# Kernel optimization log

Measured on AMD Instinct MI355X. Metric: run time of the kernel, lower is better.

The kernel has to match this reference:

```python
import jax, jax.numpy as jnp
import numpy as np


def setup_inputs() -> dict:
    key = jax.random.key(0)
    k1, k2 = jax.random.split(key)
    h = jax.random.normal(k1, (8, 16, 64, 512), dtype=jnp.float32)
    M = jax.random.normal(k2, (20000, 512), dtype=jnp.float32)
    return {"h": h, "M": M}


def reference(h, M):
    # h: [B, T, X, R], M: [K, R]
    B, T, X, R = h.shape
    hf = h.reshape(-1, R)                      # [N, R]
    att = jax.nn.softmax(hf @ M.T, axis=1)     # [N, K], unscaled dot-product
    out = att @ M                              # [N, R]
    return out.reshape(B, T, X, R)
```

## Files before the change

### kernel.cpp

```cpp
#include <hip/hip_runtime.h>
#include <stdint.h>

#define NQ 8192
#define NK 20000
#define RD 512
#define NT 157
#define TS0 79

typedef float f32x4 __attribute__((ext_vector_type(4)));
typedef short s16x8 __attribute__((ext_vector_type(8)));

__device__ __forceinline__ unsigned short bf16_rn(float x) {
    uint32_t u = __float_as_uint(x);
    return (unsigned short)((u + 0x7FFFu + ((u >> 16) & 1)) >> 16);
}

__device__ __forceinline__ void lds_barrier() {
    asm volatile("s_waitcnt lgkmcnt(0)\n\ts_barrier" ::: "memory");
}

__global__ void preconv_kernel(const float* __restrict__ M,
                               unsigned short* __restrict__ Mhi,
                               unsigned short* __restrict__ Mlo,
                               unsigned short* __restrict__ MT) {
    __shared__ float tilef[64 * 65];
    const int k0 = blockIdx.x * 64, r0 = blockIdx.y * 64;
    const int t = threadIdx.x;
#pragma unroll
    for (int i = 0; i < 16; i++) {
        int e = t + i * 256;
        int kr = e >> 6, cc = e & 63;
        int key = k0 + kr;
        if (key < NK) {
            float x = M[(size_t)key * RD + r0 + cc];
            uint32_t u = __float_as_uint(x);
            Mhi[(size_t)key * RD + r0 + cc] = (unsigned short)(u >> 16);
            Mlo[(size_t)key * RD + r0 + cc] = bf16_rn(x - __uint_as_float(u & 0xFFFF0000u));
            tilef[cc * 65 + kr] = x;
        }
    }
    __syncthreads();
#pragma unroll
    for (int i = 0; i < 16; i++) {
        int e = t + i * 256;
        int rr = e >> 6, kk = e & 63;
        int key = k0 + kk;
        if (key < NK) MT[(size_t)(r0 + rr) * NK + key] = bf16_rn(tilef[rr * 65 + kk]);
    }
}

#define S_STEP(ii, s_) do {                                                                        \
        const int sl_ = (s_) & 3;                                                                  \
        s16x8 kh0_ = kh[0][sl_], kl0_ = kl[0][sl_];                                                \
        s16x8 kh1_ = kh[1][sl_], kl1_ = kl[1][sl_];                                                \
        {                                                                                          \
            int g_ = (ii) * 16 + (s_) + 4;                                                         \
            size_t a0_ = kaddr(g_, 0), a1_ = kaddr(g_, 1);                                         \
            kh[0][sl_] = *(const s16x8*)(Mhi + a0_);                                               \
            kl[0][sl_] = *(const s16x8*)(Mlo + a0_);                                               \
            kh[1][sl_] = *(const s16x8*)(Mhi + a1_);                                               \
            kl[1][sl_] = *(const s16x8*)(Mlo + a1_);                                               \
        }                                                                                          \
        _Pragma("unroll")                                                                          \
        for (int st_ = 0; st_ < 2; st_++) {                                                        \
            s16x8 qh_ = *(const s16x8*)&qbuf[(st_ * 16 + (s_)) * 512 + l * 8];                     \
            s16x8 ql_ = *(const s16x8*)&qbuf[16384 + (st_ * 16 + (s_)) * 512 + l * 8];             \
            Cc[st_][0] = __builtin_amdgcn_mfma_f32_16x16x32_bf16(qh_, kh0_, Cc[st_][0], 0, 0, 0);  \
            Cc[st_][1] = __builtin_amdgcn_mfma_f32_16x16x32_bf16(qh_, kh1_, Cc[st_][1], 0, 0, 0);  \
            Cc[st_][0] = __builtin_amdgcn_mfma_f32_16x16x32_bf16(ql_, kh0_, Cc[st_][0], 0, 0, 0);  \
            Cc[st_][1] = __builtin_amdgcn_mfma_f32_16x16x32_bf16(ql_, kh1_, Cc[st_][1], 0, 0, 0);  \
            Cc[st_][0] = __builtin_amdgcn_mfma_f32_16x16x32_bf16(qh_, kl0_, Cc[st_][0], 0, 0, 0);  \
            Cc[st_][1] = __builtin_amdgcn_mfma_f32_16x16x32_bf16(qh_, kl1_, Cc[st_][1], 0, 0, 0);  \
        }                                                                                          \
    } while (0)

__global__ __launch_bounds__(256, 2) void flash7_kernel(
        const float* __restrict__ h,
        const unsigned short* __restrict__ Mhi,
        const unsigned short* __restrict__ Mlo,
        const unsigned short* __restrict__ MT,
        float* __restrict__ out,
        float* __restrict__ Opart,
        float* __restrict__ mpart,
        float* __restrict__ lpart,
        int nsplit) {
    __shared__ unsigned short qbuf[32768];
    __shared__ unsigned short pbuf[8 * 512];
    __shared__ float smaxb[4 * 2 * 16];
    __shared__ float ssumb[4 * 2 * 16];

    const int tid = threadIdx.x;
    const int ch = tid >> 6, l = tid & 63;
    const int l15 = l & 15, q4 = l >> 4;
    const int kq = (l15 >> 3) & 1, jj = l15 & 7;

    int qb, split;
    if (nsplit == 2) { split = blockIdx.x & 1; qb = blockIdx.x >> 1; }
    else             { split = 0;              qb = blockIdx.x; }
    const int koff = (split == 0) ? 0 : TS0 * 128;
    const int ntl  = (nsplit == 2) ? ((split == 0) ? TS0 : (NT - TS0)) : NT;
    const int total_ks = ntl * 16;
    const int qbase = qb * 32;

    const size_t base_w = (size_t)(ch * 32 + l15) * RD + q4 * 8;
    auto kaddr = [&](int g, int cb) -> size_t {
        if (g >= total_ks) g = total_ks - 1;
        int t2 = g >> 4, s2 = g & 15;
        return (size_t)(koff + t2 * 128) * RD + (size_t)s2 * 32 + base_w + (size_t)cb * (16 * RD);
    };

    s16x8 kh[2][4], kl[2][4];
#pragma unroll
    for (int i = 0; i < 4; i++) {
        size_t a0 = kaddr(i, 0), a1 = kaddr(i, 1);
        kh[0][i] = *(const s16x8*)(Mhi + a0);
        kl[0][i] = *(const s16x8*)(Mlo + a0);
        kh[1][i] = *(const s16x8*)(Mhi + a1);
        kl[1][i] = *(const s16x8*)(Mlo + a1);
    }

#pragma unroll
    for (int i = 0; i < 8; i++) {
        int g = tid + i * 256;
        int row = g >> 6, s = (g >> 2) & 15, qg = g & 3;
        int strip = row >> 4, lrow = row & 15;
        const float* src = h + (size_t)(qbase + row) * RD + s * 32 + qg * 8;
        f32x4 a = *(const f32x4*)src;
        f32x4 b = *(const f32x4*)(src + 4);
        s16x8 hi8, lo8;
#pragma unroll
        for (int j = 0; j < 8; j++) {
            float x = (j < 4) ? a[j] : b[j - 4];
            uint32_t u = __float_as_uint(x);
            hi8[j] = (short)(u >> 16);
            lo8[j] = (short)bf16_rn(x - __uint_as_float(u & 0xFFFF0000u));
        }
        int off = ((strip * 16 + s) * 512 + (qg * 16 + lrow) * 8);
        *(s16x8*)&qbuf[off] = hi8;
        *(s16x8*)&qbuf[16384 + off] = lo8;
    }
    lds_barrier();

    f32x4 O[2][8];
#pragma unroll
    for (int st = 0; st < 2; st++)
#pragma unroll
        for (int ct = 0; ct < 8; ct++) O[st][ct] = 0.f;
    f32x4 m_run[2], l_run[2];
    m_run[0] = -3e38f; m_run[1] = -3e38f; l_run[0] = 0.f; l_run[1] = 0.f;

    f32x4 Cc[2][2];
    Cc[0][0] = 0.f; Cc[0][1] = 0.f; Cc[1][0] = 0.f; Cc[1][1] = 0.f;
#pragma unroll
    for (int s = 0; s < 16; s++) S_STEP(0, s);

    for (int i = 1; i < ntl; i++) {
        const int prv = i - 1;

        f32x4 Cp[2][2];
#pragma unroll
        for (int st = 0; st < 2; st++) {
            Cp[st][0] = Cc[st][0]; Cp[st][1] = Cc[st][1];
            Cc[st][0] = 0.f;       Cc[st][1] = 0.f;
        }

        const unsigned short* mtp = MT + (size_t)(ch * 128 + l15) * NK + koff + prv * 128 + q4 * 8;
        s16x8 bt[2][4];
#pragma unroll
        for (int sk = 0; sk < 4; sk++) {
            bt[0][sk] = *(const s16x8*)(mtp + sk * 32);
            bt[1][sk] = *(const s16x8*)(mtp + (size_t)16 * NK + sk * 32);
        }
        f32x4 mx[2];
#pragma unroll
        for (int st = 0; st < 2; st++)
#pragma unroll
            for (int v = 0; v < 4; v++) mx[st][v] = fmaxf(Cp[st][0][v], Cp[st][1][v]);
#pragma unroll
        for (int d = 1; d < 16; d <<= 1) {
#pragma unroll
            for (int st = 0; st < 2; st++)
#pragma unroll
                for (int v = 0; v < 4; v++) mx[st][v] = fmaxf(mx[st][v], __shfl_xor(mx[st][v], d, 16));
        }
        if (l15 == 0) {
            *(f32x4*)&smaxb[(ch * 2 + 0) * 16 + q4 * 4] = mx[0];
            *(f32x4*)&smaxb[(ch * 2 + 1) * 16 + q4 * 4] = mx[1];
        }
#pragma unroll
        for (int s = 0; s < 5; s++) S_STEP(i, s);
        lds_barrier();

        f32x4 mnew[2]; mnew[0] = m_run[0]; mnew[1] = m_run[1];
#pragma unroll
        for (int cc = 0; cc < 4; cc++) {
#pragma unroll
            for (int st = 0; st < 2; st++) {
                f32x4 tv = *(const f32x4*)&smaxb[(cc * 2 + st) * 16 + q4 * 4];
#pragma unroll
                for (int v = 0; v < 4; v++) mnew[st][v] = fmaxf(mnew[st][v], tv[v]);
            }
        }
        f32x4 alpha[2];
#pragma unroll
        for (int st = 0; st < 2; st++)
#pragma unroll
            for (int v = 0; v < 4; v++) {
                alpha[st][v] = __expf(m_run[st][v] - mnew[st][v]);
                m_run[st][v] = mnew[st][v];
            }
        f32x4 ps[2]; ps[0] = 0.f; ps[1] = 0.f;
#pragma unroll
        for (int st = 0; st < 2; st++) {
#pragma unroll
            for (int cb = 0; cb < 2; cb++) {
#pragma unroll
                for (int v = 0; v < 4; v++) {
                    float p = __expf(Cp[st][cb][v] - mnew[st][v]);
                    ps[st][v] += p;
                    pbuf[(ch * 2 + st) * 512 + ((cb * 2 + kq) * 16 + q4 * 4 + v) * 8 + jj] = bf16_rn(p);
                }
            }
        }
#pragma unroll
        for (int d = 1; d < 16; d <<= 1) {
#pragma unroll
            for (int st = 0; st < 2; st++)
#pragma unroll
                for (int v = 0; v < 4; v++) ps[st][v] += __shfl_xor(ps[st][v], d, 16);
        }
        if (l15 == 0) {
            *(f32x4*)&ssumb[(ch * 2 + 0) * 16 + q4 * 4] = ps[0];
            *(f32x4*)&ssumb[(ch * 2 + 1) * 16 + q4 * 4] = ps[1];
        }
#pragma unroll
        for (int s = 5; s < 11; s++) S_STEP(i, s);
        lds_barrier();

        f32x4 ts[2]; ts[0] = 0.f; ts[1] = 0.f;
#pragma unroll
        for (int cc = 0; cc < 4; cc++) {
            ts[0] += *(const f32x4*)&ssumb[(cc * 2 + 0) * 16 + q4 * 4];
            ts[1] += *(const f32x4*)&ssumb[(cc * 2 + 1) * 16 + q4 * 4];
        }
#pragma unroll
        for (int st = 0; st < 2; st++)
#pragma unroll
            for (int v = 0; v < 4; v++) l_run[st][v] = l_run[st][v] * alpha[st][v] + ts[st][v];
#pragma unroll
        for (int st = 0; st < 2; st++)
#pragma unroll
            for (int ct = 0; ct < 8; ct++)
#pragma unroll
                for (int v = 0; v < 4; v++) O[st][ct][v] *= alpha[st][v];
        s16x8 pa[2][4];
#pragma unroll
        for (int st = 0; st < 2; st++)
#pragma unroll
            for (int sk = 0; sk < 4; sk++)
                pa[st][sk] = *(const s16x8*)&pbuf[((sk * 2 + st) * 512) + l * 8];
#pragma unroll
        for (int s = 11; s < 16; s++) S_STEP(i, s);
#pragma unroll
        for (int ct = 0; ct < 8; ct++) {
            s16x8 b0 = bt[ct & 1][0], b1 = bt[ct & 1][1], b2 = bt[ct & 1][2], b3 = bt[ct & 1][3];
            if (ct < 6) {
#pragma unroll
                for (int sk = 0; sk < 4; sk++)
                    bt[ct & 1][sk] = *(const s16x8*)(mtp + (size_t)(ct + 2) * 16 * NK + sk * 32);
            }
            O[0][ct] = __builtin_amdgcn_mfma_f32_16x16x32_bf16(pa[0][0], b0, O[0][ct], 0, 0, 0);
            O[1][ct] = __builtin_amdgcn_mfma_f32_16x16x32_bf16(pa[1][0], b0, O[1][ct], 0, 0, 0);
            O[0][ct] = __builtin_amdgcn_mfma_f32_16x16x32_bf16(pa[0][1], b1, O[0][ct], 0, 0, 0);
            O[1][ct] = __builtin_amdgcn_mfma_f32_16x16x32_bf16(pa[1][1], b1, O[1][ct], 0, 0, 0);
            O[0][ct] = __builtin_amdgcn_mfma_f32_16x16x32_bf16(pa[0][2], b2, O[0][ct], 0, 0, 0);
            O[1][ct] = __builtin_amdgcn_mfma_f32_16x16x32_bf16(pa[1][2], b2, O[1][ct], 0, 0, 0);
            O[0][ct] = __builtin_amdgcn_mfma_f32_16x16x32_bf16(pa[0][3], b3, O[0][ct], 0, 0, 0);
            O[1][ct] = __builtin_amdgcn_mfma_f32_16x16x32_bf16(pa[1][3], b3, O[1][ct], 0, 0, 0);
        }
    }

    {
        const int prv = ntl - 1;
#pragma unroll
        for (int cb = 0; cb < 2; cb++) {
            int kg = koff + prv * 128 + ch * 32 + cb * 16 + l15;
            if (kg >= NK) { Cc[0][cb] = -3e38f; Cc[1][cb] = -3e38f; }
        }
        const unsigned short* mtp = MT + (size_t)(ch * 128 + l15) * NK + koff + prv * 128 + q4 * 8;
        s16x8 bt[2][4];
#pragma unroll
        for (int sk = 0; sk < 4; sk++) {
            bt[0][sk] = *(const s16x8*)(mtp + sk * 32);
            bt[1][sk] = *(const s16x8*)(mtp + (size_t)16 * NK + sk * 32);
        }
        f32x4 mx[2];
#pragma unroll
        for (int st = 0; st < 2; st++)
#pragma unroll
            for (int v = 0; v < 4; v++) mx[st][v] = fmaxf(Cc[st][0][v], Cc[st][1][v]);
#pragma unroll
        for (int d = 1; d < 16; d <<= 1) {
#pragma unroll
            for (int st = 0; st < 2; st++)
#pragma unroll
                for (int v = 0; v < 4; v++) mx[st][v] = fmaxf(mx[st][v], __shfl_xor(mx[st][v], d, 16));
        }
        if (l15 == 0) {
            *(f32x4*)&smaxb[(ch * 2 + 0) * 16 + q4 * 4] = mx[0];
            *(f32x4*)&smaxb[(ch * 2 + 1) * 16 + q4 * 4] = mx[1];
        }
        lds_barrier();
        f32x4 mnew[2]; mnew[0] = m_run[0]; mnew[1] = m_run[1];
#pragma unroll
        for (int cc = 0; cc < 4; cc++) {
#pragma unroll
            for (int st = 0; st < 2; st++) {
                f32x4 tv = *(const f32x4*)&smaxb[(cc * 2 + st) * 16 + q4 * 4];
#pragma unroll
                for (int v = 0; v < 4; v++) mnew[st][v] = fmaxf(mnew[st][v], tv[v]);
            }
        }
        f32x4 alpha[2];
#pragma unroll
        for (int st = 0; st < 2; st++)
#pragma unroll
            for (int v = 0; v < 4; v++) {
                alpha[st][v] = __expf(m_run[st][v] - mnew[st][v]);
                m_run[st][v] = mnew[st][v];
            }
        f32x4 ps[2]; ps[0] = 0.f; ps[1] = 0.f;
#pragma unroll
        for (int st = 0; st < 2; st++) {
#pragma unroll
            for (int cb = 0; cb < 2; cb++) {
#pragma unroll
                for (int v = 0; v < 4; v++) {
                    float p = __expf(Cc[st][cb][v] - mnew[st][v]);
                    ps[st][v] += p;
                    pbuf[(ch * 2 + st) * 512 + ((cb * 2 + kq) * 16 + q4 * 4 + v) * 8 + jj] = bf16_rn(p);
                }
            }
        }
#pragma unroll
        for (int d = 1; d < 16; d <<= 1) {
#pragma unroll
            for (int st = 0; st < 2; st++)
#pragma unroll
                for (int v = 0; v < 4; v++) ps[st][v] += __shfl_xor(ps[st][v], d, 16);
        }
        if (l15 == 0) {
            *(f32x4*)&ssumb[(ch * 2 + 0) * 16 + q4 * 4] = ps[0];
            *(f32x4*)&ssumb[(ch * 2 + 1) * 16 + q4 * 4] = ps[1];
        }
        lds_barrier();
        f32x4 ts[2]; ts[0] = 0.f; ts[1] = 0.f;
#pragma unroll
        for (int cc = 0; cc < 4; cc++) {
            ts[0] += *(const f32x4*)&ssumb[(cc * 2 + 0) * 16 + q4 * 4];
            ts[1] += *(const f32x4*)&ssumb[(cc * 2 + 1) * 16 + q4 * 4];
        }
#pragma unroll
        for (int st = 0; st < 2; st++)
#pragma unroll
            for (int v = 0; v < 4; v++) l_run[st][v] = l_run[st][v] * alpha[st][v] + ts[st][v];
#pragma unroll
        for (int st = 0; st < 2; st++)
#pragma unroll
            for (int ct = 0; ct < 8; ct++)
#pragma unroll
                for (int v = 0; v < 4; v++) O[st][ct][v] *= alpha[st][v];
        s16x8 pa[2][4];
#pragma unroll
        for (int st = 0; st < 2; st++)
#pragma unroll
            for (int sk = 0; sk < 4; sk++)
                pa[st][sk] = *(const s16x8*)&pbuf[((sk * 2 + st) * 512) + l * 8];
#pragma unroll
        for (int ct = 0; ct < 8; ct++) {
            s16x8 b0 = bt[ct & 1][0], b1 = bt[ct & 1][1], b2 = bt[ct & 1][2], b3 = bt[ct & 1][3];
            if (ct < 6) {
#pragma unroll
                for (int sk = 0; sk < 4; sk++)
                    bt[ct & 1][sk] = *(const s16x8*)(mtp + (size_t)(ct + 2) * 16 * NK + sk * 32);
            }
            O[0][ct] = __builtin_amdgcn_mfma_f32_16x16x32_bf16(pa[0][0], b0, O[0][ct], 0, 0, 0);
            O[1][ct] = __builtin_amdgcn_mfma_f32_16x16x32_bf16(pa[1][0], b0, O[1][ct], 0, 0, 0);
            O[0][ct] = __builtin_amdgcn_mfma_f32_16x16x32_bf16(pa[0][1], b1, O[0][ct], 0, 0, 0);
            O[1][ct] = __builtin_amdgcn_mfma_f32_16x16x32_bf16(pa[1][1], b1, O[1][ct], 0, 0, 0);
            O[0][ct] = __builtin_amdgcn_mfma_f32_16x16x32_bf16(pa[0][2], b2, O[0][ct], 0, 0, 0);
            O[1][ct] = __builtin_amdgcn_mfma_f32_16x16x32_bf16(pa[1][2], b2, O[1][ct], 0, 0, 0);
            O[0][ct] = __builtin_amdgcn_mfma_f32_16x16x32_bf16(pa[0][3], b3, O[0][ct], 0, 0, 0);
            O[1][ct] = __builtin_amdgcn_mfma_f32_16x16x32_bf16(pa[1][3], b3, O[1][ct], 0, 0, 0);
        }
    }

    if (nsplit == 2) {
        float* Od = Opart + (size_t)split * NQ * RD;
#pragma unroll
        for (int st = 0; st < 2; st++)
#pragma unroll
            for (int ct = 0; ct < 8; ct++)
#pragma unroll
                for (int v = 0; v < 4; v++)
                    Od[(size_t)(qbase + st * 16 + q4 * 4 + v) * RD + ch * 128 + ct * 16 + l15] =
                        O[st][ct][v];
        if (ch == 0 && l15 == 0) {
#pragma unroll
            for (int st = 0; st < 2; st++)
#pragma unroll
                for (int v = 0; v < 4; v++) {
                    mpart[split * NQ + qbase + st * 16 + q4 * 4 + v] = m_run[st][v];
                    lpart[split * NQ + qbase + st * 16 + q4 * 4 + v] = l_run[st][v];
                }
        }
    } else {
#pragma unroll
        for (int st = 0; st < 2; st++)
#pragma unroll
            for (int ct = 0; ct < 8; ct++)
#pragma unroll
                for (int v = 0; v < 4; v++)
                    out[(size_t)(qbase + st * 16 + q4 * 4 + v) * RD + ch * 128 + ct * 16 + l15] =
                        O[st][ct][v] / l_run[st][v];
    }
}

__global__ __launch_bounds__(256) void combine_kernel(const float* __restrict__ Opart,
                                                      const float* __restrict__ mpart,
                                                      const float* __restrict__ lpart,
                                                      float* __restrict__ out) {
    const int t = threadIdx.x;
    const int row = blockIdx.x * 2 + (t >> 7);
    const int d = (t & 127) * 4;
    float m0 = mpart[row], m1 = mpart[NQ + row];
    float l0 = lpart[row], l1 = lpart[NQ + row];
    float m = fmaxf(m0, m1);
    float w0 = __expf(m0 - m), w1 = __expf(m1 - m);
    float inv = 1.f / (w0 * l0 + w1 * l1);
    f32x4 o0 = *(const f32x4*)&Opart[(size_t)row * RD + d];
    f32x4 o1 = *(const f32x4*)&Opart[(size_t)NQ * RD + (size_t)row * RD + d];
    f32x4 r;
#pragma unroll
    for (int v = 0; v < 4; v++) r[v] = (o0[v] * w0 + o1[v] * w1) * inv;
    *(f32x4*)&out[(size_t)row * RD + d] = r;
}

__global__ __launch_bounds__(256) void naive_kernel(const float* __restrict__ h,
                                                    const float* __restrict__ M,
                                                    float* __restrict__ out) {
    __shared__ float hs[16 * 520];
    __shared__ float ms[8 * 520];
    __shared__ float sdot[2][128];
    __shared__ float sm[16], sl[16], sal[16], sp[16][8];
    const int t = threadIdx.x;
    const int qbase = blockIdx.x * 16;
#pragma unroll
    for (int i = 0; i < 32; i++) {
        int e = t + i * 256;
        int row = e >> 9, col = e & 511;
        hs[row * 520 + col] = h[(size_t)(qbase + row) * RD + col];
    }
    if (t < 16) { sm[t] = -3e38f; sl[t] = 0.f; }
    float Oacc[32];
#pragma unroll
    for (int i = 0; i < 32; i++) Oacc[i] = 0.f;
    const int q = t >> 4;
    const int eb = (t & 15) * 32;

    for (int k0 = 0; k0 < NK; k0 += 8) {
        __syncthreads();
#pragma unroll
        for (int i = 0; i < 16; i++) {
            int e = t + i * 256;
            if (e < 4096) {
                int kk = e >> 9, col = e & 511;
                ms[kk * 520 + col] = M[(size_t)(k0 + kk) * RD + col];
            }
        }
        __syncthreads();
        {
            int pair = t & 127, half = t >> 7;
            int qq = pair & 15, kk = pair >> 4;
            const float* hp = &hs[qq * 520 + half * 256];
            const float* mp = &ms[kk * 520 + half * 256];
            float acc = 0.f;
#pragma unroll 8
            for (int e = 0; e < 256; e++) acc += hp[e] * mp[e];
            sdot[half][pair] = acc;
        }
        __syncthreads();
        if (t < 16) {
            int qq = t;
            float s8[8];
#pragma unroll
            for (int kk = 0; kk < 8; kk++) s8[kk] = sdot[0][qq + 16 * kk] + sdot[1][qq + 16 * kk];
            float mn = sm[qq];
#pragma unroll
            for (int kk = 0; kk < 8; kk++) mn = fmaxf(mn, s8[kk]);
            float al = __expf(sm[qq] - mn);
            float addl = 0.f;
#pragma unroll
            for (int kk = 0; kk < 8; kk++) { float p = __expf(s8[kk] - mn); sp[qq][kk] = p; addl += p; }
            sm[qq] = mn; sl[qq] = sl[qq] * al + addl; sal[qq] = al;
        }
        __syncthreads();
        {
            float al = sal[q];
#pragma unroll
            for (int i = 0; i < 32; i++) Oacc[i] *= al;
#pragma unroll
            for (int kk = 0; kk < 8; kk++) {
                float p = sp[q][kk];
                const float* mp = &ms[kk * 520 + eb];
#pragma unroll
                for (int i = 0; i < 32; i++) Oacc[i] += p * mp[i];
            }
        }
    }
    __syncthreads();
    float inv = 1.f / sl[q];
#pragma unroll
    for (int i = 0; i < 32; i++) out[(size_t)(qbase + q) * RD + eb + i] = Oacc[i] * inv;
}

extern "C" void kernel_launch(void* const* d_in, const int* in_sizes, int n_in,
                              void* d_out, int out_size, void* d_ws, size_t ws_size,
                              hipStream_t stream) {
    const float* h = (const float*)d_in[0];
    const float* M = (const float*)d_in[1];
    float* out = (float*)d_out;
    const size_t seg = (size_t)NK * RD;
    const size_t base_bytes = (seg * 3ull + 8192ull) * 2ull;
    const size_t opart_bytes = 2ull * NQ * RD * 4ull;
    const size_t stat_bytes = 2ull * 2ull * NQ * 4ull;
    const size_t need_split = base_bytes + opart_bytes + stat_bytes;

    if (ws_size >= base_bytes) {
        unsigned short* Mhi = (unsigned short*)d_ws;
        unsigned short* Mlo = Mhi + seg;
        unsigned short* MT  = Mlo + seg;
        float* Opart = (float*)((char*)d_ws + base_bytes);
        float* mpart = Opart + 2ull * NQ * RD;
        float* lpart = mpart + 2ull * NQ;
        preconv_kernel<<<dim3(313, 8), 256, 0, stream>>>(M, Mhi, Mlo, MT);
        if (ws_size >= need_split) {
            flash7_kernel<<<512, 256, 0, stream>>>(h, Mhi, Mlo, MT, out, Opart, mpart, lpart, 2);
            combine_kernel<<<NQ / 2, 256, 0, stream>>>(Opart, mpart, lpart, out);
        } else {
            flash7_kernel<<<256, 256, 0, stream>>>(h, Mhi, Mlo, MT, out, Opart, mpart, lpart, 1);
        }
    } else {
        naive_kernel<<<512, 256, 0, stream>>>(h, M, out);
    }
}
```

Baseline: 1.586 ms.

## Split flash block work across 8 wavefronts instead of 4

Doubles the block to 512 threads (8 waves). Each wave now computes one 16-key column block of S instead of two, and owns 64 output columns of O instead of 128. This halves per-wave accumulator and prefetch registers so more waves can be resident (launch bounds 512,4), which is meant to hide memory and MFMA latency. The cost is more cross-wave reductions through LDS for the row max and row sum (8 partials instead of 4), plus larger barriers.

```diff
diff --git a/kernel.cpp b/kernel.cpp
--- a/kernel.cpp
+++ b/kernel.cpp
@@ -51,30 +51,24 @@
 
 #define S_STEP(ii, s_) do {                                                                        \
         const int sl_ = (s_) & 3;                                                                  \
-        s16x8 kh0_ = kh[0][sl_], kl0_ = kl[0][sl_];                                                \
-        s16x8 kh1_ = kh[1][sl_], kl1_ = kl[1][sl_];                                                \
+        s16x8 kh0_ = kh[sl_], kl0_ = kl[sl_];                                                      \
         {                                                                                          \
             int g_ = (ii) * 16 + (s_) + 4;                                                         \
-            size_t a0_ = kaddr(g_, 0), a1_ = kaddr(g_, 1);                                         \
-            kh[0][sl_] = *(const s16x8*)(Mhi + a0_);                                               \
-            kl[0][sl_] = *(const s16x8*)(Mlo + a0_);                                               \
-            kh[1][sl_] = *(const s16x8*)(Mhi + a1_);                                               \
-            kl[1][sl_] = *(const s16x8*)(Mlo + a1_);                                               \
+            size_t a0_ = kaddr(g_);                                                                \
+            kh[sl_] = *(const s16x8*)(Mhi + a0_);                                                  \
+            kl[sl_] = *(const s16x8*)(Mlo + a0_);                                                  \
         }                                                                                          \
         _Pragma("unroll")                                                                          \
         for (int st_ = 0; st_ < 2; st_++) {                                                        \
             s16x8 qh_ = *(const s16x8*)&qbuf[(st_ * 16 + (s_)) * 512 + l * 8];                     \
             s16x8 ql_ = *(const s16x8*)&qbuf[16384 + (st_ * 16 + (s_)) * 512 + l * 8];             \
-            Cc[st_][0] = __builtin_amdgcn_mfma_f32_16x16x32_bf16(qh_, kh0_, Cc[st_][0], 0, 0, 0);  \
-            Cc[st_][1] = __builtin_amdgcn_mfma_f32_16x16x32_bf16(qh_, kh1_, Cc[st_][1], 0, 0, 0);  \
-            Cc[st_][0] = __builtin_amdgcn_mfma_f32_16x16x32_bf16(ql_, kh0_, Cc[st_][0], 0, 0, 0);  \
-            Cc[st_][1] = __builtin_amdgcn_mfma_f32_16x16x32_bf16(ql_, kh1_, Cc[st_][1], 0, 0, 0);  \
-            Cc[st_][0] = __builtin_amdgcn_mfma_f32_16x16x32_bf16(qh_, kl0_, Cc[st_][0], 0, 0, 0);  \
-            Cc[st_][1] = __builtin_amdgcn_mfma_f32_16x16x32_bf16(qh_, kl1_, Cc[st_][1], 0, 0, 0);  \
+            Cc[st_] = __builtin_amdgcn_mfma_f32_16x16x32_bf16(qh_, kh0_, Cc[st_], 0, 0, 0);        \
+            Cc[st_] = __builtin_amdgcn_mfma_f32_16x16x32_bf16(ql_, kh0_, Cc[st_], 0, 0, 0);        \
+            Cc[st_] = __builtin_amdgcn_mfma_f32_16x16x32_bf16(qh_, kl0_, Cc[st_], 0, 0, 0);        \
         }                                                                                          \
     } while (0)
 
-__global__ __launch_bounds__(256, 2) void flash7_kernel(
+__global__ __launch_bounds__(512, 4) void flash8_kernel(
         const float* __restrict__ h,
         const unsigned short* __restrict__ Mhi,
         const unsigned short* __restrict__ Mlo,
@@ -86,8 +80,8 @@
         int nsplit) {
     __shared__ unsigned short qbuf[32768];
     __shared__ unsigned short pbuf[8 * 512];
-    __shared__ float smaxb[4 * 2 * 16];
-    __shared__ float ssumb[4 * 2 * 16];
+    __shared__ float smaxb[8 * 2 * 16];
+    __shared__ float ssumb[8 * 2 * 16];
 
     const int tid = threadIdx.x;
     const int ch = tid >> 6, l = tid & 63;
@@ -102,26 +96,24 @@
     const int total_ks = ntl * 16;
     const int qbase = qb * 32;
 
-    const size_t base_w = (size_t)(ch * 32 + l15) * RD + q4 * 8;
-    auto kaddr = [&](int g, int cb) -> size_t {
+    const size_t base_w = (size_t)(ch * 16 + l15) * RD + q4 * 8;
+    auto kaddr = [&](int g) -> size_t {
         if (g >= total_ks) g = total_ks - 1;
         int t2 = g >> 4, s2 = g & 15;
-        return (size_t)(koff + t2 * 128) * RD + (size_t)s2 * 32 + base_w + (size_t)cb * (16 * RD);
+        return (size_t)(koff + t2 * 128) * RD + (size_t)s2 * 32 + base_w;
     };
 
-    s16x8 kh[2][4], kl[2][4];
+    s16x8 kh[4], kl[4];
 #pragma unroll
     for (int i = 0; i < 4; i++) {
-        size_t a0 = kaddr(i, 0), a1 = kaddr(i, 1);
-        kh[0][i] = *(const s16x8*)(Mhi + a0);
-        kl[0][i] = *(const s16x8*)(Mlo + a0);
-        kh[1][i] = *(const s16x8*)(Mhi + a1);
-        kl[1][i] = *(const s16x8*)(Mlo + a1);
-    }
-
-#pragma unroll
-    for (int i = 0; i < 8; i++) {
-        int g = tid + i * 256;
+        size_t a0 = kaddr(i);
+        kh[i] = *(const s16x8*)(Mhi + a0);
+        kl[i] = *(const s16x8*)(Mlo + a0);
+    }
+
+#pragma unroll
+    for (int i = 0; i < 4; i++) {
+        int g = tid + i * 512;
         int row = g >> 6, s = (g >> 2) & 15, qg = g & 3;
         int strip = row >> 4, lrow = row & 15;
         const float* src = h + (size_t)(qbase + row) * RD + s * 32 + qg * 8;
@@ -141,30 +133,27 @@
     }
     lds_barrier();
 
-    f32x4 O[2][8];
+    f32x4 O[2][4];
 #pragma unroll
     for (int st = 0; st < 2; st++)
 #pragma unroll
-        for (int ct = 0; ct < 8; ct++) O[st][ct] = 0.f;
+        for (int ct = 0; ct < 4; ct++) O[st][ct] = 0.f;
     f32x4 m_run[2], l_run[2];
     m_run[0] = -3e38f; m_run[1] = -3e38f; l_run[0] = 0.f; l_run[1] = 0.f;
 
-    f32x4 Cc[2][2];
-    Cc[0][0] = 0.f; Cc[0][1] = 0.f; Cc[1][0] = 0.f; Cc[1][1] = 0.f;
+    f32x4 Cc[2];
+    Cc[0] = 0.f; Cc[1] = 0.f;
 #pragma unroll
     for (int s = 0; s < 16; s++) S_STEP(0, s);
 
     for (int i = 1; i < ntl; i++) {
         const int prv = i - 1;
 
-        f32x4 Cp[2][2];
-#pragma unroll
-        for (int st = 0; st < 2; st++) {
-            Cp[st][0] = Cc[st][0]; Cp[st][1] = Cc[st][1];
-            Cc[st][0] = 0.f;       Cc[st][1] = 0.f;
-        }
-
-        const unsigned short* mtp = MT + (size_t)(ch * 128 + l15) * NK + koff + prv * 128 + q4 * 8;
+        f32x4 Cp[2];
+        Cp[0] = Cc[0]; Cp[1] = Cc[1];
+        Cc[0] = 0.f;   Cc[1] = 0.f;
+
+        const unsigned short* mtp = MT + (size_t)(ch * 64 + l15) * NK + koff + prv * 128 + q4 * 8;
         s16x8 bt[2][4];
 #pragma unroll
         for (int sk = 0; sk < 4; sk++) {
@@ -175,7 +164,7 @@
 #pragma unroll
         for (int st = 0; st < 2; st++)
 #pragma unroll
-            for (int v = 0; v < 4; v++) mx[st][v] = fmaxf(Cp[st][0][v], Cp[st][1][v]);
+            for (int v = 0; v < 4; v++) mx[st][v] = Cp[st][v];
 #pragma unroll
         for (int d = 1; d < 16; d <<= 1) {
 #pragma unroll
@@ -193,7 +182,7 @@
 
         f32x4 mnew[2]; mnew[0] = m_run[0]; mnew[1] = m_run[1];
 #pragma unroll
-        for (int cc = 0; cc < 4; cc++) {
+        for (int cc = 0; cc < 8; cc++) {
 #pragma unroll
             for (int st = 0; st < 2; st++) {
                 f32x4 tv = *(const f32x4*)&smaxb[(cc * 2 + st) * 16 + q4 * 4];
@@ -213,13 +202,11 @@
 #pragma unroll
         for (int st = 0; st < 2; st++) {
 #pragma unroll
-            for (int cb = 0; cb < 2; cb++) {
-#pragma unroll
-                for (int v = 0; v < 4; v++) {
-                    float p = __expf(Cp[st][cb][v] - mnew[st][v]);
-                    ps[st][v] += p;
-                    pbuf[(ch * 2 + st) * 512 + ((cb * 2 + kq) * 16 + q4 * 4 + v) * 8 + jj] = bf16_rn(p);
-                }
+            for (int v = 0; v < 4; v++) {
+                float p = __expf(Cp[st][v] - mnew[st][v]);
+                ps[st][v] += p;
+                pbuf[((ch >> 1) * 2 + st) * 512 +
+                     ((((ch & 1) * 2 + kq) * 16) + q4 * 4 + v) * 8 + jj] = bf16_rn(p);
             }
         }
 #pragma unroll
@@ -239,7 +226,7 @@
 
         f32x4 ts[2]; ts[0] = 0.f; ts[1] = 0.f;
 #pragma unroll
-        for (int cc = 0; cc < 4; cc++) {
+        for (int cc = 0; cc < 8; cc++) {
             ts[0] += *(const f32x4*)&ssumb[(cc * 2 + 0) * 16 + q4 * 4];
             ts[1] += *(const f32x4*)&ssumb[(cc * 2 + 1) * 16 + q4 * 4];
         }
@@ -250,7 +237,7 @@
 #pragma unroll
         for (int st = 0; st < 2; st++)
 #pragma unroll
-            for (int ct = 0; ct < 8; ct++)
+            for (int ct = 0; ct < 4; ct++)
 #pragma unroll
                 for (int v = 0; v < 4; v++) O[st][ct][v] *= alpha[st][v];
         s16x8 pa[2][4];
@@ -262,9 +249,9 @@
 #pragma unroll
         for (int s = 11; s < 16; s++) S_STEP(i, s);
 #pragma unroll
-        for (int ct = 0; ct < 8; ct++) {
+        for (int ct = 0; ct < 4; ct++) {
             s16x8 b0 = bt[ct & 1][0], b1 = bt[ct & 1][1], b2 = bt[ct & 1][2], b3 = bt[ct & 1][3];
-            if (ct < 6) {
+            if (ct < 2) {
 #pragma unroll
                 for (int sk = 0; sk < 4; sk++)
                     bt[ct & 1][sk] = *(const s16x8*)(mtp + (size_t)(ct + 2) * 16 * NK + sk * 32);
@@ -282,12 +269,11 @@
 
     {
         const int prv = ntl - 1;
-#pragma unroll
-        for (int cb = 0; cb < 2; cb++) {
-            int kg = koff + prv * 128 + ch * 32 + cb * 16 + l15;
-            if (kg >= NK) { Cc[0][cb] = -3e38f; Cc[1][cb] = -3e38f; }
-        }
-        const unsigned short* mtp = MT + (size_t)(ch * 128 + l15) * NK + koff + prv * 128 + q4 * 8;
+        {
+            int kg = koff + prv * 128 + ch * 16 + l15;
+            if (kg >= NK) { Cc[0] = -3e38f; Cc[1] = -3e38f; }
+        }
+        const unsigned short* mtp = MT + (size_t)(ch * 64 + l15) * NK + koff + prv * 128 + q4 * 8;
         s16x8 bt[2][4];
 #pragma unroll
         for (int sk = 0; sk < 4; sk++) {
@@ -298,7 +284,7 @@
 #pragma unroll
         for (int st = 0; st < 2; st++)
 #pragma unroll
-            for (int v = 0; v < 4; v++) mx[st][v] = fmaxf(Cc[st][0][v], Cc[st][1][v]);
+            for (int v = 0; v < 4; v++) mx[st][v] = Cc[st][v];
 #pragma unroll
         for (int d = 1; d < 16; d <<= 1) {
 #pragma unroll
@@ -313,7 +299,7 @@
         lds_barrier();
         f32x4 mnew[2]; mnew[0] = m_run[0]; mnew[1] = m_run[1];
 #pragma unroll
-        for (int cc = 0; cc < 4; cc++) {
+        for (int cc = 0; cc < 8; cc++) {
 #pragma unroll
             for (int st = 0; st < 2; st++) {
                 f32x4 tv = *(const f32x4*)&smaxb[(cc * 2 + st) * 16 + q4 * 4];
@@ -333,13 +319,11 @@
 #pragma unroll
         for (int st = 0; st < 2; st++) {
 #pragma unroll
-            for (int cb = 0; cb < 2; cb++) {
-#pragma unroll
-                for (int v = 0; v < 4; v++) {
-                    float p = __expf(Cc[st][cb][v] - mnew[st][v]);
-                    ps[st][v] += p;
-                    pbuf[(ch * 2 + st) * 512 + ((cb * 2 + kq) * 16 + q4 * 4 + v) * 8 + jj] = bf16_rn(p);
-                }
+            for (int v = 0; v < 4; v++) {
+                float p = __expf(Cc[st][v] - mnew[st][v]);
+                ps[st][v] += p;
+                pbuf[((ch >> 1) * 2 + st) * 512 +
+                     ((((ch & 1) * 2 + kq) * 16) + q4 * 4 + v) * 8 + jj] = bf16_rn(p);
             }
         }
 #pragma unroll
@@ -356,7 +340,7 @@
         lds_barrier();
         f32x4 ts[2]; ts[0] = 0.f; ts[1] = 0.f;
 #pragma unroll
-        for (int cc = 0; cc < 4; cc++) {
+        for (int cc = 0; cc < 8; cc++) {
             ts[0] += *(const f32x4*)&ssumb[(cc * 2 + 0) * 16 + q4 * 4];
             ts[1] += *(const f32x4*)&ssumb[(cc * 2 + 1) * 16 + q4 * 4];
         }
@@ -367,7 +351,7 @@
 #pragma unroll
         for (int st = 0; st < 2; st++)
 #pragma unroll
-            for (int ct = 0; ct < 8; ct++)
+            for (int ct = 0; ct < 4; ct++)
 #pragma unroll
                 for (int v = 0; v < 4; v++) O[st][ct][v] *= alpha[st][v];
         s16x8 pa[2][4];
@@ -377,9 +361,9 @@
             for (int sk = 0; sk < 4; sk++)
                 pa[st][sk] = *(const s16x8*)&pbuf[((sk * 2 + st) * 512) + l * 8];
 #pragma unroll
-        for (int ct = 0; ct < 8; ct++) {
+        for (int ct = 0; ct < 4; ct++) {
             s16x8 b0 = bt[ct & 1][0], b1 = bt[ct & 1][1], b2 = bt[ct & 1][2], b3 = bt[ct & 1][3];
-            if (ct < 6) {
+            if (ct < 2) {
 #pragma unroll
                 for (int sk = 0; sk < 4; sk++)
                     bt[ct & 1][sk] = *(const s16x8*)(mtp + (size_t)(ct + 2) * 16 * NK + sk * 32);
@@ -400,10 +384,10 @@
 #pragma unroll
         for (int st = 0; st < 2; st++)
 #pragma unroll
-            for (int ct = 0; ct < 8; ct++)
+            for (int ct = 0; ct < 4; ct++)
 #pragma unroll
                 for (int v = 0; v < 4; v++)
-                    Od[(size_t)(qbase + st * 16 + q4 * 4 + v) * RD + ch * 128 + ct * 16 + l15] =
+                    Od[(size_t)(qbase + st * 16 + q4 * 4 + v) * RD + ch * 64 + ct * 16 + l15] =
                         O[st][ct][v];
         if (ch == 0 && l15 == 0) {
 #pragma unroll
@@ -418,10 +402,10 @@
 #pragma unroll
         for (int st = 0; st < 2; st++)
 #pragma unroll
-            for (int ct = 0; ct < 8; ct++)
+            for (int ct = 0; ct < 4; ct++)
 #pragma unroll
                 for (int v = 0; v < 4; v++)
-                    out[(size_t)(qbase + st * 16 + q4 * 4 + v) * RD + ch * 128 + ct * 16 + l15] =
+                    out[(size_t)(qbase + st * 16 + q4 * 4 + v) * RD + ch * 64 + ct * 16 + l15] =
                         O[st][ct][v] / l_run[st][v];
     }
 }
@@ -545,10 +529,10 @@
         float* lpart = mpart + 2ull * NQ;
         preconv_kernel<<<dim3(313, 8), 256, 0, stream>>>(M, Mhi, Mlo, MT);
         if (ws_size >= need_split) {
-            flash7_kernel<<<512, 256, 0, stream>>>(h, Mhi, Mlo, MT, out, Opart, mpart, lpart, 2);
+            flash8_kernel<<<512, 512, 0, stream>>>(h, Mhi, Mlo, MT, out, Opart, mpart, lpart, 2);
             combine_kernel<<<NQ / 2, 256, 0, stream>>>(Opart, mpart, lpart, out);
         } else {
-            flash7_kernel<<<256, 256, 0, stream>>>(h, Mhi, Mlo, MT, out, Opart, mpart, lpart, 1);
+            flash8_kernel<<<256, 512, 0, stream>>>(h, Mhi, Mlo, MT, out, Opart, mpart, lpart, 1);
         }
     } else {
         naive_kernel<<<512, 256, 0, stream>>>(h, M, out);
```

Result: slower. 2.315 ms (+46.0%).
